# Kernel optimization log

Measured on AMD Instinct MI355X. Metric: run time of the kernel, lower is better.

Reference implementation:

```python
import jax, jax.numpy as jnp
import numpy as np

B, L, D = 4, 4096, 768
ORDER = 2
EMB = 33      # HyenaFilter emb_dim default
FFN = 64      # filter_order
FREQ = 10.0


def setup_inputs() -> dict:
    key = jax.random.key(0)
    ks = jax.random.split(key, 10)
    def rn(i, shape, scale):
        return jax.random.normal(ks[i], shape, dtype=jnp.float32) * scale
    return {
        "u": jax.random.normal(ks[0], (B, L, D), dtype=jnp.float32),
        "W_in": rn(1, (D, (ORDER + 1) * D), 0.02),
        "b_in": jnp.zeros(((ORDER + 1) * D,), jnp.float32),
        "conv_k": rn(2, (3, (ORDER + 1) * D), 0.3),   # depthwise kernel, 3 taps
        "conv_b": jnp.zeros(((ORDER + 1) * D,), jnp.float32),
        "W1": rn(3, (EMB, FFN), 0.1),
        "b1": jnp.zeros((FFN,), jnp.float32),
        "W2": rn(4, (FFN, ORDER * D), 0.05),
        "b2": jnp.zeros((ORDER * D,), jnp.float32),
        "f_bias": rn(5, (ORDER, D), 0.05),
        "f_decay": rn(6, (ORDER, D), 0.05),
        "W_out": rn(7, (D, D), 0.02),
        "b_out": jnp.zeros((D,), jnp.float32),
    }


def _hyena_filter(W1, b1, W2, b2, f_bias, f_decay):
    # Implicit filter: sinusoidal positional features -> MLP with sin activation
    t = jnp.linspace(0.0, 1.0, L)[:, None]                      # [L,1]
    bands = jnp.linspace(0.0, float(EMB - 1), EMB)[None, :]     # [1,EMB]
    pe = jnp.sin(t * bands * FREQ)                              # [L,EMB]
    h = jnp.sin(FREQ * (pe @ W1 + b1))                          # [L,FFN]
    h = h @ W2 + b2                                             # [L,ORDER*D]
    h = h.reshape(L, ORDER, D).transpose(1, 2, 0)               # [ORDER,D,L]
    t_window = jnp.linspace(0.0, float(L), L)[None, None, :]    # [1,1,L]
    decay = jnp.exp(-jnp.exp(f_decay)[:, :, None] * t_window)   # [ORDER,D,L]
    return h * decay + f_bias[:, :, None]


def reference(u, W_in, b_in, conv_k, conv_b, W1, b1, W2, b2,
              f_bias, f_decay, W_out, b_out):
    # input projection: [B,L,D] -> [B,L,(ORDER+1)*D]
    proj = u @ W_in + b_in
    # depthwise causal conv, kernel_size=3 (pad 2 on the left)
    xp = jnp.pad(proj, ((0, 0), (2, 0), (0, 0)))
    proj = (xp[:, 0:L, :] * conv_k[0]
            + xp[:, 1:L + 1, :] * conv_k[1]
            + xp[:, 2:L + 2, :] * conv_k[2]) + conv_b
    proj = proj.reshape(B, L, ORDER + 1, D).transpose(0, 2, 3, 1)  # [B,ORDER+1,D,L]
    x = proj[:, :ORDER]   # gates, [B,ORDER,D,L]
    v = proj[:, ORDER]    # value, [B,D,L]

    h = _hyena_filter(W1, b1, W2, b2, f_bias, f_decay)  # [ORDER,D,L]

    n_fft = 2 * L  # zero-padded linear convolution via rfft
    for n in range(ORDER):
        v_f = jnp.fft.rfft(v, n=n_fft, axis=-1)          # [B,D,L+1] complex
        h_f = jnp.fft.rfft(h[n], n=n_fft, axis=-1)       # [D,L+1] complex
        y = jnp.fft.irfft(v_f * h_f[None], n=n_fft, axis=-1)[..., :L]
        v = y * x[:, n]                                   # gated recurrence

    return v.transpose(0, 2, 1) @ W_out + b_out           # [B,L,D]
```

## Files before the change

kernel.cpp:

```cpp
#include <hip/hip_runtime.h>
#include <math.h>

#define L_SEQ 4096
#define D_DIM 768
#define C3    2304
#define TAPS  32

typedef __attribute__((ext_vector_type(8))) short bf16x8;
typedef __attribute__((ext_vector_type(4))) float f32x4;

__device__ __forceinline__ unsigned short f2bf(float x) {
  union { float f; unsigned u; } v; v.f = x;
  unsigned r = v.u + 0x7FFF + ((v.u >> 16) & 1);
  return (unsigned short)(r >> 16);
}
__device__ __forceinline__ float bf2f(unsigned short u) {
  union { unsigned u; float f; } v; v.u = ((unsigned)u) << 16; return v.f;
}
__device__ __forceinline__ void gld_lds16(const void* g, void* l) {
  __builtin_amdgcn_global_load_lds((const __attribute__((address_space(1))) void*)g,
                                   (__attribute__((address_space(3))) void*)l, 16, 0, 0);
}

__global__ __launch_bounds__(256) void filt_kernel(const float* __restrict__ W1,
                                                   const float* __restrict__ b1,
                                                   const float* __restrict__ W2,
                                                   const float* __restrict__ b2,
                                                   const float* __restrict__ f_decay,
                                                   float* __restrict__ g_tab) {
  __shared__ float phi_s[2048];
  const int tid = threadIdx.x;
  #pragma unroll
  for (int it = 0; it < 8; ++it) {
    int idx = tid + it * 256;
    int t = idx >> 6, f = idx & 63;
    float tt = (float)t / 4095.0f;
    float s = b1[f];
    #pragma unroll
    for (int e = 0; e < 33; ++e)
      s += sinf(tt * (float)e * 10.0f) * W1[e * 64 + f];
    phi_s[idx] = sinf(10.0f * s);
  }
  __syncthreads();
  int idx = blockIdx.x * 256 + tid;
  int c2 = idx >> 5, t = idx & 31;
  float acc = b2[c2];
  #pragma unroll 8
  for (int f = 0; f < 64; ++f)
    acc += phi_s[t * 64 + f] * W2[f * 1536 + c2];
  float r = expf(f_decay[c2]);
  g_tab[idx] = acc * expf(-r * (float)t * (4096.0f / 4095.0f));
}

__global__ __launch_bounds__(256) void cvt_kernel(const float* __restrict__ src,
                                                  unsigned short* __restrict__ dst) {
  int idx = (blockIdx.x * 256 + threadIdx.x) * 4;
  float4 v = *(const float4*)&src[idx];
  ushort4 o;
  o.x = f2bf(v.x); o.y = f2bf(v.y); o.z = f2bf(v.z); o.w = f2bf(v.w);
  *(ushort4*)&dst[idx] = o;
}

__global__ __launch_bounds__(256) void wtrans_kernel(const float* __restrict__ W_in,
                                                     unsigned short* __restrict__ W_inT,
                                                     const float* __restrict__ W_out,
                                                     unsigned short* __restrict__ W_outT) {
  __shared__ float t[32][33];
  const int z = blockIdx.z;
  const float* src = z ? W_out : W_in;
  unsigned short* dst = z ? W_outT : W_inT;
  const int C = z ? 768 : 2304;
  const int c0 = blockIdx.x * 32, r0 = blockIdx.y * 32;
  if (c0 >= C) return;
  const int tx = threadIdx.x & 31, ty = threadIdx.x >> 5;
  #pragma unroll
  for (int rr = 0; rr < 4; ++rr)
    t[ty + rr * 8][tx] = src[(long)(r0 + ty + rr * 8) * C + c0 + tx];
  __syncthreads();
  #pragma unroll
  for (int rr = 0; rr < 4; ++rr)
    dst[(long)(c0 + ty + rr * 8) * 768 + r0 + tx] = f2bf(t[tx][ty + rr * 8]);
}

__device__ __forceinline__ void g_vmwait(int VM) {
  if (VM == 4)      asm volatile("s_waitcnt vmcnt(4)" ::: "memory");
  else if (VM == 0) asm volatile("s_waitcnt vmcnt(0)" ::: "memory");
}

template<bool STG, int VM>
__device__ __forceinline__ void g_step(int scur, int sstg, int kt, char* smemc, int tid,
                                       int wm64, int wn64, int fm, int csel,
                                       const unsigned short* aP, const unsigned short* bP,
                                       f32x4 (&acc)[4][4]) {
  const unsigned short* As = (const unsigned short*)(smemc + scur * 16384);
  const unsigned short* Bs = (const unsigned short*)(smemc + scur * 16384 + 8192);
  bf16x8 af[4], bfr[4];
  #pragma unroll
  for (int i = 0; i < 4; ++i) af[i]  = *(const bf16x8*)&As[(wm64 + i * 16 + fm) * 32 + csel];
  #pragma unroll
  for (int jj = 0; jj < 4; ++jj) bfr[jj] = *(const bf16x8*)&Bs[(wn64 + jj * 16 + fm) * 32 + csel];
  if (STG) {
    const unsigned short* ap = aP + (kt + 2) * 32;
    const unsigned short* bp = bP + (kt + 2) * 32;
    char* d = smemc + sstg * 16384 + tid * 16;
    gld_lds16(ap,         d);
    gld_lds16(ap + 49152, d + 4096);
    gld_lds16(bp,         d + 8192);
    gld_lds16(bp + 49152, d + 12288);
  }
  asm volatile("" ::: "memory");
  __builtin_amdgcn_s_barrier();
  __builtin_amdgcn_s_setprio(1);
  __builtin_amdgcn_sched_barrier(0);
  #pragma unroll
  for (int i = 0; i < 4; ++i)
    #pragma unroll
    for (int jj = 0; jj < 4; ++jj)
      acc[i][jj] = __builtin_amdgcn_mfma_f32_16x16x32_bf16(af[i], bfr[jj], acc[i][jj], 0, 0, 0);
  __builtin_amdgcn_sched_barrier(0);
  __builtin_amdgcn_s_setprio(0);
  g_vmwait(VM);
  asm volatile("" ::: "memory");
  __builtin_amdgcn_s_barrier();
}

__device__ __forceinline__ void g_kloop(char* smemc, int tid, int wm64, int wn64, int fm,
                                        int csel, const unsigned short* aP,
                                        const unsigned short* bP, f32x4 (&acc)[4][4]) {
  #pragma unroll
  for (int kt = 0; kt < 2; ++kt) {
    char* d = smemc + kt * 16384 + tid * 16;
    const unsigned short* ap = aP + kt * 32;
    const unsigned short* bp = bP + kt * 32;
    gld_lds16(ap,         d);
    gld_lds16(ap + 49152, d + 4096);
    gld_lds16(bp,         d + 8192);
    gld_lds16(bp + 49152, d + 12288);
  }
  asm volatile("s_waitcnt vmcnt(4)" ::: "memory");
  asm volatile("" ::: "memory");
  __builtin_amdgcn_s_barrier();
  int scur = 0;
  #pragma unroll 1
  for (int kt = 0; kt < 22; ++kt) {
    int sstg = scur + 2; if (sstg >= 3) sstg -= 3;
    g_step<true, 4>(scur, sstg, kt, smemc, tid, wm64, wn64, fm, csel, aP, bP, acc);
    scur = (scur == 2) ? 0 : scur + 1;
  }
  {
    int sstg = scur + 2; if (sstg >= 3) sstg -= 3;
    g_step<false, 0>(scur, sstg, 22, smemc, tid, wm64, wn64, fm, csel, aP, bP, acc);
    scur = (scur == 2) ? 0 : scur + 1;
  }
  g_step<false, -1>(scur, 0, 23, smemc, tid, wm64, wn64, fm, csel, aP, bP, acc);
}

__global__ __launch_bounds__(256, 3) void gemm1_k3(const unsigned short* __restrict__ A,
                                                   const unsigned short* __restrict__ Bt,
                                                   const float* __restrict__ bias,
                                                   unsigned short* __restrict__ proj) {
  extern __shared__ char smemc[];
  const int tid = threadIdx.x;
  const int w = tid >> 6, lane = tid & 63;
  const int id = blockIdx.x;
  const int x8 = id & 7, jb = id >> 3;
  const int mt = x8 * 16 + jb / 18, nt = jb % 18;
  const int m0 = mt * 128, n0 = nt * 128;
  const int wm64 = (w & 1) * 64, wn64 = (w >> 1) * 64;
  const int fm = lane & 15;
  const int csel = (((lane >> 4) ^ ((fm >> 1) & 3)) << 3);
  const int q_src = ((tid & 3) ^ ((tid >> 3) & 3)) * 8;
  const unsigned short* aP = A  + (size_t)(m0 + (tid >> 2)) * 768 + q_src;
  const unsigned short* bP = Bt + (size_t)(n0 + (tid >> 2)) * 768 + q_src;
  f32x4 acc[4][4] = {};
  g_kloop(smemc, tid, wm64, wn64, fm, csel, aP, bP, acc);

  const int b = m0 >> 12, l0 = m0 & 4095;
  float* fbuf = (float*)smemc + w * 1088;
  const int fk = lane >> 4;
  #pragma unroll
  for (int j2 = 0; j2 < 4; ++j2) {
    __syncthreads();
    #pragma unroll
    for (int i = 0; i < 4; ++i)
      *(f32x4*)&fbuf[fm * 68 + i * 16 + fk * 4] = acc[i][j2];
    __syncthreads();
    #pragma unroll
    for (int p = 0; p < 4; ++p) {
      int nl = p * 4 + fk;
      int c = n0 + wn64 + j2 * 16 + nl;
      float4 v = *(float4*)&fbuf[nl * 68 + fm * 4];
      float bb = bias[c];
      ushort4 o;
      o.x = f2bf(v.x + bb); o.y = f2bf(v.y + bb);
      o.z = f2bf(v.z + bb); o.w = f2bf(v.w + bb);
      *(ushort4*)&proj[((size_t)b * C3 + c) * L_SEQ + l0 + wm64 + fm * 4] = o;
    }
  }
}

__global__ __launch_bounds__(256, 3) void gemm2_k3(const unsigned short* __restrict__ A,
                                                   const unsigned short* __restrict__ Bt,
                                                   const float* __restrict__ bias,
                                                   float* __restrict__ out) {
  extern __shared__ char smemc[];
  const int tid = threadIdx.x;
  const int w = tid >> 6, lane = tid & 63;
  const int id = blockIdx.x;
  const int x8 = id & 7, jb = id >> 3;
  const int mt = x8 * 16 + jb / 6, nt = jb % 6;
  const int m0 = mt * 128, n0 = nt * 128;
  const int wm64 = (w & 1) * 64, wn64 = (w >> 1) * 64;
  const int fm = lane & 15;
  const int csel = (((lane >> 4) ^ ((fm >> 1) & 3)) << 3);
  const int q_src = ((tid & 3) ^ ((tid >> 3) & 3)) * 8;
  const unsigned short* aP = A  + (size_t)(m0 + (tid >> 2)) * 768 + q_src;
  const unsigned short* bP = Bt + (size_t)(n0 + (tid >> 2)) * 768 + q_src;
  f32x4 acc[4][4] = {};
  g_kloop(smemc, tid, wm64, wn64, fm, csel, aP, bP, acc);

  float* fbuf = (float*)smemc + w * 1088;
  const int fk = lane >> 4;
  const int nf = lane & 15, mq = lane >> 4;
  float4 bb4 = *(const float4*)&bias[n0 + wn64 + nf * 4];
  #pragma unroll
  for (int i = 0; i < 4; ++i) {
    __syncthreads();
    #pragma unroll
    for (int cg = 0; cg < 4; ++cg)
      #pragma unroll
      for (int r = 0; r < 4; ++r)
        fbuf[(fk * 4 + r) * 68 + cg * 16 + fm] = acc[i][cg][r];
    __syncthreads();
    #pragma unroll
    for (int pass = 0; pass < 4; ++pass) {
      int m_l = pass * 4 + mq;
      float4 v = *(float4*)&fbuf[m_l * 68 + nf * 4];
      v.x += bb4.x; v.y += bb4.y; v.z += bb4.z; v.w += bb4.w;
      *(float4*)&out[(size_t)(m0 + wm64 + i * 16 + m_l) * D_DIM + n0 + wn64 + nf * 4] = v;
    }
  }
}

__global__ __launch_bounds__(256) void row_kernel(const unsigned short* __restrict__ proj,
                                                  unsigned short* __restrict__ v2T,
                                                  const float* __restrict__ conv_k,
                                                  const float* __restrict__ conv_b,
                                                  const float* __restrict__ g_tab,
                                                  const float* __restrict__ f_bias) {
  __shared__ float buf0[4128];
  __shared__ float buf1[4128];
  __shared__ float sgs[2 * TAPS];
  __shared__ float wsum[4];
  __shared__ float bnd[3][4][2];
  const int tid = threadIdx.x;
  const int lane = tid & 63, w = tid >> 6;
  const int b = blockIdx.x / D_DIM, d = blockIdx.x % D_DIM;
  const int g = tid * 16;

  const unsigned short* rowV  = proj + ((size_t)b * C3 + 2 * D_DIM + d) * L_SEQ;
  const unsigned short* rowX0 = proj + ((size_t)b * C3 + d) * L_SEQ;
  const unsigned short* rowX1 = proj + ((size_t)b * C3 + D_DIM + d) * L_SEQ;

  float v[16], x0[16], x1[16];
  #pragma unroll
  for (int k = 0; k < 4; ++k) {
    ushort4 qv = *(const ushort4*)&rowV[g + k * 4];
    v[k * 4] = bf2f(qv.x); v[k * 4 + 1] = bf2f(qv.y); v[k * 4 + 2] = bf2f(qv.z); v[k * 4 + 3] = bf2f(qv.w);
    ushort4 q0 = *(const ushort4*)&rowX0[g + k * 4];
    x0[k * 4] = bf2f(q0.x); x0[k * 4 + 1] = bf2f(q0.y); x0[k * 4 + 2] = bf2f(q0.z); x0[k * 4 + 3] = bf2f(q0.w);
    ushort4 q1 = *(const ushort4*)&rowX1[g + k * 4];
    x1[k * 4] = bf2f(q1.x); x1[k * 4 + 1] = bf2f(q1.y); x1[k * 4 + 2] = bf2f(q1.z); x1[k * 4 + 3] = bf2f(q1.w);
  }

  if (tid < 32) {
    int ph = (tid & 15) * 258 + (tid >> 4);
    buf0[ph] = 0.f; buf1[ph] = 0.f;
  }
  if (tid < 64) sgs[tid] = g_tab[((size_t)((tid >> 5) * D_DIM + d)) * TAPS + (tid & 31)];
  if (lane == 63) {
    bnd[0][w][0] = v[14];  bnd[0][w][1] = v[15];
    bnd[1][w][0] = x0[14]; bnd[1][w][1] = x0[15];
    bnd[2][w][0] = x1[14]; bnd[2][w][1] = x1[15];
  }
  const int cv = 2 * D_DIM + d, cx0 = d, cx1 = D_DIM + d;
  const float kv0 = conv_k[cv],  kv1 = conv_k[C3 + cv],  kv2 = conv_k[2 * C3 + cv],  bv = conv_b[cv];
  const float ka0 = conv_k[cx0], ka1 = conv_k[C3 + cx0], ka2 = conv_k[2 * C3 + cx0], ba = conv_b[cx0];
  const float kb0 = conv_k[cx1], kb1 = conv_k[C3 + cx1], kb2 = conv_k[2 * C3 + cx1], bb = conv_b[cx1];
  const float fb0 = f_bias[d], fb1 = f_bias[D_DIM + d];
  __syncthreads();

  float vm1 = __shfl_up(v[15], 1),  vm2 = __shfl_up(v[14], 1);
  float am1 = __shfl_up(x0[15], 1), am2 = __shfl_up(x0[14], 1);
  float bm1 = __shfl_up(x1[15], 1), bm2 = __shfl_up(x1[14], 1);
  if (lane == 0) {
    if (w > 0) {
      vm2 = bnd[0][w-1][0]; vm1 = bnd[0][w-1][1];
      am2 = bnd[1][w-1][0]; am1 = bnd[1][w-1][1];
      bm2 = bnd[2][w-1][0]; bm1 = bnd[2][w-1][1];
    } else {
      vm1 = vm2 = am1 = am2 = bm1 = bm2 = 0.f;
    }
  }
  float r[16];
  r[0] = vm2 * kv0 + vm1 * kv1 + v[0] * kv2 + bv;
  r[1] = vm1 * kv0 + v[0] * kv1 + v[1] * kv2 + bv;
  #pragma unroll
  for (int i = 2; i < 16; ++i) r[i] = v[i-2] * kv0 + v[i-1] * kv1 + v[i] * kv2 + bv;
  {
    float t0 = am2 * ka0 + am1 * ka1 + x0[0] * ka2 + ba;
    float t1 = am1 * ka0 + x0[0] * ka1 + x0[1] * ka2 + ba;
    #pragma unroll
    for (int i = 15; i >= 2; --i) x0[i] = x0[i-2] * ka0 + x0[i-1] * ka1 + x0[i] * ka2 + ba;
    x0[0] = t0; x0[1] = t1;
  }
  {
    float t0 = bm2 * kb0 + bm1 * kb1 + x1[0] * kb2 + bb;
    float t1 = bm1 * kb0 + x1[0] * kb1 + x1[1] * kb2 + bb;
    #pragma unroll
    for (int i = 15; i >= 2; --i) x1[i] = x1[i-2] * kb0 + x1[i-1] * kb1 + x1[i] * kb2 + bb;
    x1[0] = t0; x1[1] = t1;
  }
  #pragma unroll
  for (int i = 0; i < 16; ++i) buf0[i * 258 + tid + 2] = r[i];
  __syncthreads();

  float h[32];
  #pragma unroll
  for (int j = 0; j < 32; ++j) h[j] = buf0[(j & 15) * 258 + tid + (j >> 4)];
  float p[16], run = 0.f;
  #pragma unroll
  for (int i = 0; i < 16; ++i) { run += r[i]; p[i] = run; }
  float s = run;
  #pragma unroll
  for (int off = 1; off < 64; off <<= 1) {
    float o = __shfl_up(s, off);
    if (lane >= off) s += o;
  }
  if (lane == 63) wsum[w] = s;
  __syncthreads();
  float woff = 0.f;
  #pragma unroll
  for (int k = 0; k < 4; ++k) if (k < w) woff += wsum[k];
  float excl = woff + s - run;
  float y0[16];
  #pragma unroll
  for (int i = 0; i < 16; ++i) {
    float a = fb0 * (excl + p[i]);
    #pragma unroll
    for (int t = 0; t < TAPS; ++t) {
      float vv = (t <= i) ? r[i - t] : h[32 + i - t];
      a += sgs[t] * vv;
    }
    y0[i] = a * x0[i];
  }
  #pragma unroll
  for (int i = 0; i < 16; ++i) buf1[i * 258 + tid + 2] = y0[i];
  __syncthreads();

  #pragma unroll
  for (int j = 0; j < 32; ++j) h[j] = buf1[(j & 15) * 258 + tid + (j >> 4)];
  run = 0.f;
  #pragma unroll
  for (int i = 0; i < 16; ++i) { run += y0[i]; p[i] = run; }
  s = run;
  #pragma unroll
  for (int off = 1; off < 64; off <<= 1) {
    float o = __shfl_up(s, off);
    if (lane >= off) s += o;
  }
  if (lane == 63) wsum[w] = s;
  __syncthreads();
  woff = 0.f;
  #pragma unroll
  for (int k = 0; k < 4; ++k) if (k < w) woff += wsum[k];
  excl = woff + s - run;
  unsigned short yout[16];
  #pragma unroll
  for (int i = 0; i < 16; ++i) {
    float a = fb1 * (excl + p[i]);
    #pragma unroll
    for (int t = 0; t < TAPS; ++t) {
      float vv = (t <= i) ? y0[i - t] : h[32 + i - t];
      a += sgs[TAPS + t] * vv;
    }
    yout[i] = f2bf(a * x1[i]);
  }
  unsigned short* outRow = v2T + ((size_t)b * D_DIM + d) * L_SEQ + g;
  *(ushort4*)&outRow[0]  = *(ushort4*)&yout[0];
  *(ushort4*)&outRow[4]  = *(ushort4*)&yout[4];
  *(ushort4*)&outRow[8]  = *(ushort4*)&yout[8];
  *(ushort4*)&outRow[12] = *(ushort4*)&yout[12];
}

__global__ __launch_bounds__(256) void transpose_v2(const unsigned short* __restrict__ src,
                                                    unsigned short* __restrict__ dst) {
  __shared__ unsigned short t[64][66];
  const int l0 = blockIdx.x * 64, d0 = blockIdx.y * 64, b = blockIdx.z;
  const int tx = threadIdx.x & 31, ty = threadIdx.x >> 5;
  const unsigned short* s = src + ((size_t)b * D_DIM + d0) * L_SEQ + l0;
  #pragma unroll
  for (int r = 0; r < 8; ++r) {
    int dd = ty + r * 8;
    *(ushort2*)&t[dd][tx * 2] = *(const ushort2*)&s[(size_t)dd * L_SEQ + tx * 2];
  }
  __syncthreads();
  unsigned short* q = dst + ((size_t)b * L_SEQ + l0) * D_DIM + d0;
  #pragma unroll
  for (int r = 0; r < 8; ++r) {
    int ll = ty + r * 8;
    ushort2 v; v.x = t[tx * 2][ll]; v.y = t[tx * 2 + 1][ll];
    *(ushort2*)&q[(size_t)ll * D_DIM + tx * 2] = v;
  }
}

extern "C" void kernel_launch(void* const* d_in, const int* in_sizes, int n_in,
                              void* d_out, int out_size, void* d_ws, size_t ws_size,
                              hipStream_t stream) {
  (void)in_sizes; (void)n_in; (void)out_size; (void)ws_size;
  const float* u       = (const float*)d_in[0];
  const float* W_in    = (const float*)d_in[1];
  const float* b_in    = (const float*)d_in[2];
  const float* conv_k  = (const float*)d_in[3];
  const float* conv_b  = (const float*)d_in[4];
  const float* W1      = (const float*)d_in[5];
  const float* b1      = (const float*)d_in[6];
  const float* W2      = (const float*)d_in[7];
  const float* b2      = (const float*)d_in[8];
  const float* f_bias  = (const float*)d_in[9];
  const float* f_decay = (const float*)d_in[10];
  const float* W_out   = (const float*)d_in[11];
  const float* b_out   = (const float*)d_in[12];
  float* out = (float*)d_out;

  unsigned short* proj  = (unsigned short*)d_ws;
  unsigned short* v2T   = proj + (size_t)4 * C3 * L_SEQ;
  unsigned short* ubf   = v2T + (size_t)4 * D_DIM * L_SEQ;
  unsigned short* v2F   = ubf;
  unsigned short* W_inT = ubf + (size_t)16384 * 768;
  unsigned short* W_outT= W_inT + (size_t)C3 * D_DIM;
  float* g_tab          = (float*)(W_outT + (size_t)D_DIM * D_DIM);

  static bool g_attr = false;
  if (!g_attr) {
    (void)hipFuncSetAttribute(reinterpret_cast<const void*>(gemm1_k3),
                              hipFuncAttributeMaxDynamicSharedMemorySize, 49152);
    (void)hipFuncSetAttribute(reinterpret_cast<const void*>(gemm2_k3),
                              hipFuncAttributeMaxDynamicSharedMemorySize, 49152);
    g_attr = true;
  }

  filt_kernel<<<192, 256, 0, stream>>>(W1, b1, W2, b2, f_decay, g_tab);
  cvt_kernel<<<12288, 256, 0, stream>>>(u, ubf);
  wtrans_kernel<<<dim3(72, 24, 2), 256, 0, stream>>>(W_in, W_inT, W_out, W_outT);
  gemm1_k3<<<2304, 256, 49152, stream>>>(ubf, W_inT, b_in, proj);
  row_kernel<<<3072, 256, 0, stream>>>(proj, v2T, conv_k, conv_b, g_tab, f_bias);
  transpose_v2<<<dim3(64, 12, 4), 256, 0, stream>>>(v2T, v2F);
  gemm2_k3<<<768, 256, 49152, stream>>>(v2F, W_outT, b_out, out);
}
```

Measured before the change: 289.5 us.

## Fuse prep kernels and retile input GEMM to 256x128 with 512 threads

```diff
diff --git a/kernel.cpp b/kernel.cpp
--- a/kernel.cpp
+++ b/kernel.cpp
@@ -21,65 +21,186 @@
   __builtin_amdgcn_global_load_lds((const __attribute__((address_space(1))) void*)g,
                                    (__attribute__((address_space(3))) void*)l, 16, 0, 0);
 }
-
-__global__ __launch_bounds__(256) void filt_kernel(const float* __restrict__ W1,
+__device__ __forceinline__ void lds_fence() {
+  asm volatile("s_waitcnt lgkmcnt(0)" ::: "memory");
+  __builtin_amdgcn_sched_barrier(0);
+}
+
+__global__ __launch_bounds__(256) void prep_kernel(const float* __restrict__ u,
+                                                   unsigned short* __restrict__ ubf,
+                                                   const float* __restrict__ W_in,
+                                                   unsigned short* __restrict__ W_inT,
+                                                   const float* __restrict__ W_out,
+                                                   unsigned short* __restrict__ W_outT,
+                                                   const float* __restrict__ W1,
                                                    const float* __restrict__ b1,
                                                    const float* __restrict__ W2,
                                                    const float* __restrict__ b2,
                                                    const float* __restrict__ f_decay,
                                                    float* __restrict__ g_tab) {
-  __shared__ float phi_s[2048];
+  __shared__ float sh[2048];
+  const int bid = blockIdx.x;
   const int tid = threadIdx.x;
-  #pragma unroll
-  for (int it = 0; it < 8; ++it) {
-    int idx = tid + it * 256;
-    int t = idx >> 6, f = idx & 63;
-    float tt = (float)t / 4095.0f;
-    float s = b1[f];
-    #pragma unroll
-    for (int e = 0; e < 33; ++e)
-      s += sinf(tt * (float)e * 10.0f) * W1[e * 64 + f];
-    phi_s[idx] = sinf(10.0f * s);
-  }
-  __syncthreads();
-  int idx = blockIdx.x * 256 + tid;
-  int c2 = idx >> 5, t = idx & 31;
-  float acc = b2[c2];
-  #pragma unroll 8
-  for (int f = 0; f < 64; ++f)
-    acc += phi_s[t * 64 + f] * W2[f * 1536 + c2];
-  float r = expf(f_decay[c2]);
-  g_tab[idx] = acc * expf(-r * (float)t * (4096.0f / 4095.0f));
-}
-
-__global__ __launch_bounds__(256) void cvt_kernel(const float* __restrict__ src,
-                                                  unsigned short* __restrict__ dst) {
-  int idx = (blockIdx.x * 256 + threadIdx.x) * 4;
-  float4 v = *(const float4*)&src[idx];
-  ushort4 o;
-  o.x = f2bf(v.x); o.y = f2bf(v.y); o.z = f2bf(v.z); o.w = f2bf(v.w);
-  *(ushort4*)&dst[idx] = o;
-}
-
-__global__ __launch_bounds__(256) void wtrans_kernel(const float* __restrict__ W_in,
-                                                     unsigned short* __restrict__ W_inT,
-                                                     const float* __restrict__ W_out,
-                                                     unsigned short* __restrict__ W_outT) {
-  __shared__ float t[32][33];
-  const int z = blockIdx.z;
-  const float* src = z ? W_out : W_in;
-  unsigned short* dst = z ? W_outT : W_inT;
-  const int C = z ? 768 : 2304;
-  const int c0 = blockIdx.x * 32, r0 = blockIdx.y * 32;
-  if (c0 >= C) return;
-  const int tx = threadIdx.x & 31, ty = threadIdx.x >> 5;
-  #pragma unroll
-  for (int rr = 0; rr < 4; ++rr)
-    t[ty + rr * 8][tx] = src[(long)(r0 + ty + rr * 8) * C + c0 + tx];
-  __syncthreads();
-  #pragma unroll
-  for (int rr = 0; rr < 4; ++rr)
-    dst[(long)(c0 + ty + rr * 8) * 768 + r0 + tx] = f2bf(t[tx][ty + rr * 8]);
+  if (bid < 12288) {
+    int idx = (bid * 256 + tid) * 4;
+    float4 v = *(const float4*)&u[idx];
+    ushort4 o;
+    o.x = f2bf(v.x); o.y = f2bf(v.y); o.z = f2bf(v.z); o.w = f2bf(v.w);
+    *(ushort4*)&ubf[idx] = o;
+  } else if (bid < 14592) {
+    float (*t)[33] = (float(*)[33])sh;
+    int id = bid - 12288;
+    const int z = (id >= 1728) ? 1 : 0;
+    if (z) id -= 1728;
+    const int nx = z ? 24 : 72;
+    const int bx = id % nx, by = id / nx;
+    const float* src = z ? W_out : W_in;
+    unsigned short* dst = z ? W_outT : W_inT;
+    const int C = z ? 768 : 2304;
+    const int c0 = bx * 32, r0 = by * 32;
+    const int tx = tid & 31, ty = tid >> 5;
+    #pragma unroll
+    for (int rr = 0; rr < 4; ++rr)
+      t[ty + rr * 8][tx] = src[(long)(r0 + ty + rr * 8) * C + c0 + tx];
+    __syncthreads();
+    #pragma unroll
+    for (int rr = 0; rr < 4; ++rr)
+      dst[(long)(c0 + ty + rr * 8) * 768 + r0 + tx] = f2bf(t[tx][ty + rr * 8]);
+  } else {
+    float* phi_s = sh;
+    const int fb = bid - 14592;
+    #pragma unroll
+    for (int it = 0; it < 8; ++it) {
+      int idx = tid + it * 256;
+      int t = idx >> 6, f = idx & 63;
+      float tt = (float)t / 4095.0f;
+      float s = b1[f];
+      #pragma unroll
+      for (int e = 0; e < 33; ++e)
+        s += sinf(tt * (float)e * 10.0f) * W1[e * 64 + f];
+      phi_s[idx] = sinf(10.0f * s);
+    }
+    __syncthreads();
+    int idx = fb * 256 + tid;
+    int c2 = idx >> 5, t = idx & 31;
+    float acc = b2[c2];
+    #pragma unroll 8
+    for (int f = 0; f < 64; ++f)
+      acc += phi_s[t * 64 + f] * W2[f * 1536 + c2];
+    float r = expf(f_decay[c2]);
+    g_tab[idx] = acc * expf(-r * (float)t * (4096.0f / 4095.0f));
+  }
+}
+
+__device__ __forceinline__ void g1_vmwait(int VM) {
+  if (VM == 3)      asm volatile("s_waitcnt vmcnt(3)" ::: "memory");
+  else if (VM == 0) asm volatile("s_waitcnt vmcnt(0)" ::: "memory");
+}
+
+template<bool STG, int VM>
+__device__ __forceinline__ void g1_step(int scur, int sstg, int kt, char* smemc, int tid,
+                                        int wmRow, int wn64, int fm, int csel,
+                                        const unsigned short* aP, const unsigned short* bP,
+                                        f32x4 (&acc)[4][4]) {
+  const unsigned short* As = (const unsigned short*)(smemc + scur * 24576);
+  const unsigned short* Bs = (const unsigned short*)(smemc + scur * 24576 + 16384);
+  bf16x8 af[4], bfr[4];
+  #pragma unroll
+  for (int i = 0; i < 4; ++i) af[i]  = *(const bf16x8*)&As[(wmRow + i * 16 + fm) * 32 + csel];
+  #pragma unroll
+  for (int jj = 0; jj < 4; ++jj) bfr[jj] = *(const bf16x8*)&Bs[(wn64 + jj * 16 + fm) * 32 + csel];
+  if (STG) {
+    const unsigned short* ap = aP + (kt + 2) * 32;
+    const unsigned short* bp = bP + (kt + 2) * 32;
+    char* d = smemc + sstg * 24576 + tid * 16;
+    gld_lds16(ap,         d);
+    gld_lds16(ap + 98304, d + 8192);
+    gld_lds16(bp,         d + 16384);
+  }
+  asm volatile("" ::: "memory");
+  __builtin_amdgcn_s_barrier();
+  __builtin_amdgcn_s_setprio(1);
+  __builtin_amdgcn_sched_barrier(0);
+  #pragma unroll
+  for (int i = 0; i < 4; ++i)
+    #pragma unroll
+    for (int jj = 0; jj < 4; ++jj)
+      acc[i][jj] = __builtin_amdgcn_mfma_f32_16x16x32_bf16(af[i], bfr[jj], acc[i][jj], 0, 0, 0);
+  __builtin_amdgcn_sched_barrier(0);
+  __builtin_amdgcn_s_setprio(0);
+  g1_vmwait(VM);
+  asm volatile("" ::: "memory");
+  __builtin_amdgcn_s_barrier();
+}
+
+__global__ __launch_bounds__(512, 4) void gemm1_2ph(const unsigned short* __restrict__ A,
+                                                    const unsigned short* __restrict__ Bt,
+                                                    const float* __restrict__ bias,
+                                                    unsigned short* __restrict__ proj) {
+  extern __shared__ char smemc[];
+  const int tid = threadIdx.x;
+  const int w = tid >> 6, lane = tid & 63;
+  const int id = blockIdx.x;
+  const int x8 = id & 7, jb = id >> 3;
+  const int mt = x8 * 8 + jb / 18, nt = jb % 18;
+  const int m0 = mt * 256, n0 = nt * 128;
+  const int wmRow = (w & 3) * 64, wn64 = (w >> 2) * 64;
+  const int fm = lane & 15;
+  const int csel = (((lane >> 4) ^ ((fm >> 1) & 3)) << 3);
+  const int q_src = ((tid & 3) ^ ((tid >> 3) & 3)) * 8;
+  const unsigned short* aP = A  + (size_t)(m0 + (tid >> 2)) * 768 + q_src;
+  const unsigned short* bP = Bt + (size_t)(n0 + (tid >> 2)) * 768 + q_src;
+  f32x4 acc[4][4] = {};
+
+  #pragma unroll
+  for (int kt = 0; kt < 2; ++kt) {
+    char* d = smemc + kt * 24576 + tid * 16;
+    const unsigned short* ap = aP + kt * 32;
+    const unsigned short* bp = bP + kt * 32;
+    gld_lds16(ap,         d);
+    gld_lds16(ap + 98304, d + 8192);
+    gld_lds16(bp,         d + 16384);
+  }
+  asm volatile("s_waitcnt vmcnt(3)" ::: "memory");
+  asm volatile("" ::: "memory");
+  __builtin_amdgcn_s_barrier();
+
+  int scur = 0;
+  #pragma unroll 1
+  for (int kt = 0; kt < 22; ++kt) {
+    int sstg = scur + 2; if (sstg >= 3) sstg -= 3;
+    g1_step<true, 3>(scur, sstg, kt, smemc, tid, wmRow, wn64, fm, csel, aP, bP, acc);
+    scur = (scur == 2) ? 0 : scur + 1;
+  }
+  {
+    int sstg = scur + 2; if (sstg >= 3) sstg -= 3;
+    g1_step<false, 0>(scur, sstg, 22, smemc, tid, wmRow, wn64, fm, csel, aP, bP, acc);
+    scur = (scur == 2) ? 0 : scur + 1;
+  }
+  g1_step<false, -1>(scur, 0, 23, smemc, tid, wmRow, wn64, fm, csel, aP, bP, acc);
+
+  const int b = m0 >> 12, l0 = m0 & 4095;
+  float* fbuf = (float*)smemc + w * 1088;
+  const int fk = lane >> 4;
+  #pragma unroll
+  for (int j2 = 0; j2 < 4; ++j2) {
+    #pragma unroll
+    for (int i = 0; i < 4; ++i)
+      *(f32x4*)&fbuf[fm * 68 + i * 16 + fk * 4] = acc[i][j2];
+    lds_fence();
+    #pragma unroll
+    for (int p = 0; p < 4; ++p) {
+      int nl = p * 4 + fk;
+      int c = n0 + wn64 + j2 * 16 + nl;
+      float4 v = *(float4*)&fbuf[nl * 68 + fm * 4];
+      float bb = bias[c];
+      ushort4 o;
+      o.x = f2bf(v.x + bb); o.y = f2bf(v.y + bb);
+      o.z = f2bf(v.z + bb); o.w = f2bf(v.w + bb);
+      *(ushort4*)&proj[((size_t)b * C3 + c) * L_SEQ + l0 + wmRow + fm * 4] = o;
+    }
+    lds_fence();
+  }
 }
 
 __device__ __forceinline__ void g_vmwait(int VM) {
@@ -122,81 +243,6 @@
   g_vmwait(VM);
   asm volatile("" ::: "memory");
   __builtin_amdgcn_s_barrier();
-}
-
-__device__ __forceinline__ void g_kloop(char* smemc, int tid, int wm64, int wn64, int fm,
-                                        int csel, const unsigned short* aP,
-                                        const unsigned short* bP, f32x4 (&acc)[4][4]) {
-  #pragma unroll
-  for (int kt = 0; kt < 2; ++kt) {
-    char* d = smemc + kt * 16384 + tid * 16;
-    const unsigned short* ap = aP + kt * 32;
-    const unsigned short* bp = bP + kt * 32;
-    gld_lds16(ap,         d);
-    gld_lds16(ap + 49152, d + 4096);
-    gld_lds16(bp,         d + 8192);
-    gld_lds16(bp + 49152, d + 12288);
-  }
-  asm volatile("s_waitcnt vmcnt(4)" ::: "memory");
-  asm volatile("" ::: "memory");
-  __builtin_amdgcn_s_barrier();
-  int scur = 0;
-  #pragma unroll 1
-  for (int kt = 0; kt < 22; ++kt) {
-    int sstg = scur + 2; if (sstg >= 3) sstg -= 3;
-    g_step<true, 4>(scur, sstg, kt, smemc, tid, wm64, wn64, fm, csel, aP, bP, acc);
-    scur = (scur == 2) ? 0 : scur + 1;
-  }
-  {
-    int sstg = scur + 2; if (sstg >= 3) sstg -= 3;
-    g_step<false, 0>(scur, sstg, 22, smemc, tid, wm64, wn64, fm, csel, aP, bP, acc);
-    scur = (scur == 2) ? 0 : scur + 1;
-  }
-  g_step<false, -1>(scur, 0, 23, smemc, tid, wm64, wn64, fm, csel, aP, bP, acc);
-}
-
-__global__ __launch_bounds__(256, 3) void gemm1_k3(const unsigned short* __restrict__ A,
-                                                   const unsigned short* __restrict__ Bt,
-                                                   const float* __restrict__ bias,
-                                                   unsigned short* __restrict__ proj) {
-  extern __shared__ char smemc[];
-  const int tid = threadIdx.x;
-  const int w = tid >> 6, lane = tid & 63;
-  const int id = blockIdx.x;
-  const int x8 = id & 7, jb = id >> 3;
-  const int mt = x8 * 16 + jb / 18, nt = jb % 18;
-  const int m0 = mt * 128, n0 = nt * 128;
-  const int wm64 = (w & 1) * 64, wn64 = (w >> 1) * 64;
-  const int fm = lane & 15;
-  const int csel = (((lane >> 4) ^ ((fm >> 1) & 3)) << 3);
-  const int q_src = ((tid & 3) ^ ((tid >> 3) & 3)) * 8;
-  const unsigned short* aP = A  + (size_t)(m0 + (tid >> 2)) * 768 + q_src;
-  const unsigned short* bP = Bt + (size_t)(n0 + (tid >> 2)) * 768 + q_src;
-  f32x4 acc[4][4] = {};
-  g_kloop(smemc, tid, wm64, wn64, fm, csel, aP, bP, acc);
-
-  const int b = m0 >> 12, l0 = m0 & 4095;
-  float* fbuf = (float*)smemc + w * 1088;
-  const int fk = lane >> 4;
-  #pragma unroll
-  for (int j2 = 0; j2 < 4; ++j2) {
-    __syncthreads();
-    #pragma unroll
-    for (int i = 0; i < 4; ++i)
-      *(f32x4*)&fbuf[fm * 68 + i * 16 + fk * 4] = acc[i][j2];
-    __syncthreads();
-    #pragma unroll
-    for (int p = 0; p < 4; ++p) {
-      int nl = p * 4 + fk;
-      int c = n0 + wn64 + j2 * 16 + nl;
-      float4 v = *(float4*)&fbuf[nl * 68 + fm * 4];
-      float bb = bias[c];
-      ushort4 o;
-      o.x = f2bf(v.x + bb); o.y = f2bf(v.y + bb);
-      o.z = f2bf(v.z + bb); o.w = f2bf(v.w + bb);
-      *(ushort4*)&proj[((size_t)b * C3 + c) * L_SEQ + l0 + wm64 + fm * 4] = o;
-    }
-  }
 }
 
 __global__ __launch_bounds__(256, 3) void gemm2_k3(const unsigned short* __restrict__ A,
@@ -217,7 +263,33 @@
   const unsigned short* aP = A  + (size_t)(m0 + (tid >> 2)) * 768 + q_src;
   const unsigned short* bP = Bt + (size_t)(n0 + (tid >> 2)) * 768 + q_src;
   f32x4 acc[4][4] = {};
-  g_kloop(smemc, tid, wm64, wn64, fm, csel, aP, bP, acc);
+
+  #pragma unroll
+  for (int kt = 0; kt < 2; ++kt) {
+    char* d = smemc + kt * 16384 + tid * 16;
+    const unsigned short* ap = aP + kt * 32;
+    const unsigned short* bp = bP + kt * 32;
+    gld_lds16(ap,         d);
+    gld_lds16(ap + 49152, d + 4096);
+    gld_lds16(bp,         d + 8192);
+    gld_lds16(bp + 49152, d + 12288);
+  }
+  asm volatile("s_waitcnt vmcnt(4)" ::: "memory");
+  asm volatile("" ::: "memory");
+  __builtin_amdgcn_s_barrier();
+  int scur = 0;
+  #pragma unroll 1
+  for (int kt = 0; kt < 22; ++kt) {
+    int sstg = scur + 2; if (sstg >= 3) sstg -= 3;
+    g_step<true, 4>(scur, sstg, kt, smemc, tid, wm64, wn64, fm, csel, aP, bP, acc);
+    scur = (scur == 2) ? 0 : scur + 1;
+  }
+  {
+    int sstg = scur + 2; if (sstg >= 3) sstg -= 3;
+    g_step<false, 0>(scur, sstg, 22, smemc, tid, wm64, wn64, fm, csel, aP, bP, acc);
+    scur = (scur == 2) ? 0 : scur + 1;
+  }
+  g_step<false, -1>(scur, 0, 23, smemc, tid, wm64, wn64, fm, csel, aP, bP, acc);
 
   float* fbuf = (float*)smemc + w * 1088;
   const int fk = lane >> 4;
@@ -225,13 +297,12 @@
   float4 bb4 = *(const float4*)&bias[n0 + wn64 + nf * 4];
   #pragma unroll
   for (int i = 0; i < 4; ++i) {
-    __syncthreads();
     #pragma unroll
     for (int cg = 0; cg < 4; ++cg)
       #pragma unroll
       for (int r = 0; r < 4; ++r)
         fbuf[(fk * 4 + r) * 68 + cg * 16 + fm] = acc[i][cg][r];
-    __syncthreads();
+    lds_fence();
     #pragma unroll
     for (int pass = 0; pass < 4; ++pass) {
       int m_l = pass * 4 + mq;
@@ -239,6 +310,7 @@
       v.x += bb4.x; v.y += bb4.y; v.z += bb4.z; v.w += bb4.w;
       *(float4*)&out[(size_t)(m0 + wm64 + i * 16 + m_l) * D_DIM + n0 + wn64 + nf * 4] = v;
     }
+    lds_fence();
   }
 }
 
@@ -443,17 +515,16 @@
 
   static bool g_attr = false;
   if (!g_attr) {
-    (void)hipFuncSetAttribute(reinterpret_cast<const void*>(gemm1_k3),
-                              hipFuncAttributeMaxDynamicSharedMemorySize, 49152);
+    (void)hipFuncSetAttribute(reinterpret_cast<const void*>(gemm1_2ph),
+                              hipFuncAttributeMaxDynamicSharedMemorySize, 73728);
     (void)hipFuncSetAttribute(reinterpret_cast<const void*>(gemm2_k3),
                               hipFuncAttributeMaxDynamicSharedMemorySize, 49152);
     g_attr = true;
   }
 
-  filt_kernel<<<192, 256, 0, stream>>>(W1, b1, W2, b2, f_decay, g_tab);
-  cvt_kernel<<<12288, 256, 0, stream>>>(u, ubf);
-  wtrans_kernel<<<dim3(72, 24, 2), 256, 0, stream>>>(W_in, W_inT, W_out, W_outT);
-  gemm1_k3<<<2304, 256, 49152, stream>>>(ubf, W_inT, b_in, proj);
+  prep_kernel<<<14784, 256, 0, stream>>>(u, ubf, W_in, W_inT, W_out, W_outT,
+                                         W1, b1, W2, b2, f_decay, g_tab);
+  gemm1_2ph<<<1152, 512, 73728, stream>>>(ubf, W_inT, b_in, proj);
   row_kernel<<<3072, 256, 0, stream>>>(proj, v2T, conv_k, conv_b, g_tab, f_bias);
   transpose_v2<<<dim3(64, 12, 4), 256, 0, stream>>>(v2T, v2F);
   gemm2_k3<<<768, 256, 49152, stream>>>(v2F, W_outT, b_out, out);
```

Result: no change. 292.5 us (+1.0%).
